# Kernel optimization log

Hardware: AMD Instinct MI355X
Metric: run time of the kernel (lower is better)

Reference implementation:

```python
import jax, jax.numpy as jnp
import numpy as np

BIG = 1e9  # self-distance masking constant, as in the torch module


def setup_inputs() -> dict:
    key = jax.random.key(0)
    k1, _ = jax.random.split(key)
    coords = jax.random.normal(k1, (8, 4096, 3), dtype=jnp.float32)
    mask = jnp.ones((8, 4096), dtype=bool)
    return {"coords": coords, "mask": mask}


def reference(coords, mask):
    # coords: [B, N, 3]; mask is accepted but unused (matches the torch module)
    B, N, _ = coords.shape
    # Pairwise Euclidean distances via the |a|^2 + |b|^2 - 2ab identity
    # (avoids materializing the [B,N,N,3] diff tensor the torch code builds).
    sq = jnp.sum(coords * coords, axis=-1)                      # [B, N]
    inner = jnp.einsum('bnd,bmd->bnm', coords, coords)          # [B, N, N]
    d2 = sq[:, :, None] + sq[:, None, :] - 2.0 * inner
    dist = jnp.sqrt(jnp.maximum(d2, 0.0))                       # [B, N, N]
    dist = dist + jnp.eye(N, dtype=dist.dtype) * BIG            # mask self
    # argsort(dim=2)[:, :, :2] == indices of the two smallest distances
    _, idx = jax.lax.top_k(-dist, 2)                            # [B, N, 2]
    first_nearest_indices = idx[:, :, 0]
    second_nearest_indices = idx[:, :, 1]
    A = jnp.take_along_axis(
        coords, jnp.broadcast_to(first_nearest_indices[:, :, None], (B, N, 3)), axis=1)
    C = jnp.take_along_axis(
        coords, jnp.broadcast_to(second_nearest_indices[:, :, None], (B, N, 3)), axis=1)
    return (A, C, first_nearest_indices, second_nearest_indices)
```

## Files before the change

kernel.cpp:

```cpp
#include <hip/hip_runtime.h>

#define BATCH 8
#define NPTS 4096
#define TOTQ (BATCH * NPTS)
#define TPB 256
#define BIGD 1e30f

__device__ __forceinline__ void top2min(float k, int m,
                                        float& b1, int& i1,
                                        float& b2, int& i2) {
    bool c1 = k < b1;
    bool c2 = k < b2;
    int ni2 = c2 ? m : i2;
    i2 = c1 ? i1 : ni2;
    i1 = c1 ? m : i1;
    b2 = fminf(fmaxf(k, b1), b2);
    b1 = fminf(k, b1);
}

template <int CHUNKSZ, int Q, bool EXC>
__device__ __forceinline__ void scan_loop(const float4* __restrict__ pts, int mbase,
                                          const int* nq,
                                          const float* xn, const float* yn, const float* zn,
                                          float* b1, int* i1, float* b2, int* i2) {
    for (int p = 0; p < CHUNKSZ; p += 8) {
        float4 c[8];
#pragma unroll
        for (int j = 0; j < 8; ++j) c[j] = pts[p + j];
#pragma unroll
        for (int j = 0; j < 8; ++j) {
            const int m = mbase + p + j;
#pragma unroll
            for (int q = 0; q < Q; ++q) {
                float k = fmaf(c[j].x, xn[q], fmaf(c[j].y, yn[q], fmaf(c[j].z, zn[q], c[j].w)));
                if (EXC) k = (m == nq[q]) ? BIGD : k;
                top2min(k, m, b1[q], i1[q], b2[q], i2[q]);
            }
        }
    }
}

template <int NCHUNKS, int Q>
__global__ __launch_bounds__(TPB) void knn_scan(const float* __restrict__ coords,
                                                float4* __restrict__ partial) {
    constexpr int CHUNKSZ = NPTS / NCHUNKS;
    __shared__ float4 pts[CHUNKSZ];
    const int tid   = (int)threadIdx.x;
    const int tile  = blockIdx.x;
    const int chunk = blockIdx.y;
    const int b     = blockIdx.z;
    const float* cb = coords + (size_t)b * NPTS * 3;
    const int mbase = chunk * CHUNKSZ;

    for (int p = tid; p < CHUNKSZ; p += TPB) {
        float x = cb[(mbase + p) * 3 + 0];
        float y = cb[(mbase + p) * 3 + 1];
        float z = cb[(mbase + p) * 3 + 2];
        pts[p] = make_float4(-2.0f * x, -2.0f * y, -2.0f * z, x * x + y * y + z * z);
    }

    const int qbase = tile * (TPB * Q);
    int nq[Q];
    float xn[Q], yn[Q], zn[Q], b1[Q], b2[Q];
    int i1[Q], i2[Q];
#pragma unroll
    for (int q = 0; q < Q; ++q) {
        int n = qbase + q * TPB + tid;
        nq[q] = n;
        xn[q] = cb[n * 3 + 0];
        yn[q] = cb[n * 3 + 1];
        zn[q] = cb[n * 3 + 2];
        b1[q] = BIGD; b2[q] = BIGD; i1[q] = 0; i2[q] = 0;
    }
    __syncthreads();

    const int qend = qbase + TPB * Q;
    const int mend = mbase + CHUNKSZ;
    if (mbase < qend && qbase < mend) {
        scan_loop<CHUNKSZ, Q, true >(pts, mbase, nq, xn, yn, zn, b1, i1, b2, i2);
    } else {
        scan_loop<CHUNKSZ, Q, false>(pts, mbase, nq, xn, yn, zn, b1, i1, b2, i2);
    }

#pragma unroll
    for (int q = 0; q < Q; ++q) {
        int n = qbase + q * TPB + tid;
        partial[(size_t)chunk * TOTQ + (size_t)b * NPTS + n] =
            make_float4(b1[q], __int_as_float(i1[q]), b2[q], __int_as_float(i2[q]));
    }
}

template <int NCHUNKS>
__global__ __launch_bounds__(TPB) void knn_merge(const float* __restrict__ coords,
                                                 const float4* __restrict__ partial,
                                                 float* __restrict__ out) {
    const int q = blockIdx.x * TPB + (int)threadIdx.x;
    const int b = q >> 12;
    float b1 = BIGD, b2 = BIGD;
    int i1 = 0, i2 = 0;
#pragma unroll
    for (int c = 0; c < NCHUNKS; ++c) {
        float4 pc = partial[(size_t)c * TOTQ + q];
        top2min(pc.x, __float_as_int(pc.y), b1, i1, b2, i2);
        top2min(pc.z, __float_as_int(pc.w), b1, i1, b2, i2);
    }
    const float* cb = coords + (size_t)b * NPTS * 3;
    float* A  = out;
    float* C  = out + (size_t)TOTQ * 3;
    float* I1 = out + (size_t)2 * TOTQ * 3;
    float* I2 = I1 + (size_t)TOTQ;

    A[(size_t)q * 3 + 0] = cb[i1 * 3 + 0];
    A[(size_t)q * 3 + 1] = cb[i1 * 3 + 1];
    A[(size_t)q * 3 + 2] = cb[i1 * 3 + 2];
    C[(size_t)q * 3 + 0] = cb[i2 * 3 + 0];
    C[(size_t)q * 3 + 1] = cb[i2 * 3 + 1];
    C[(size_t)q * 3 + 2] = cb[i2 * 3 + 2];
    I1[q] = (float)i1;
    I2[q] = (float)i2;
}

__global__ __launch_bounds__(TPB) void knn_full(const float* __restrict__ coords,
                                                float* __restrict__ out) {
    __shared__ float4 pts[NPTS];
    const int tid  = (int)threadIdx.x;
    const int tile = blockIdx.x;
    const int b    = blockIdx.y;
    const float* cb = coords + (size_t)b * NPTS * 3;

    for (int p = tid; p < NPTS; p += TPB) {
        float x = cb[p * 3 + 0];
        float y = cb[p * 3 + 1];
        float z = cb[p * 3 + 2];
        pts[p] = make_float4(-2.0f * x, -2.0f * y, -2.0f * z, x * x + y * y + z * z);
    }
    const int n = tile * TPB + tid;
    const float xn = cb[n * 3 + 0];
    const float yn = cb[n * 3 + 1];
    const float zn = cb[n * 3 + 2];
    __syncthreads();

    float b1 = BIGD, b2 = BIGD;
    int i1 = 0, i2 = 0;
    for (int p = 0; p < NPTS; p += 4) {
#pragma unroll
        for (int j = 0; j < 4; ++j) {
            float4 c = pts[p + j];
            float k = fmaf(c.x, xn, fmaf(c.y, yn, fmaf(c.z, zn, c.w)));
            k = (p + j == n) ? BIGD : k;
            top2min(k, p + j, b1, i1, b2, i2);
        }
    }

    const int q = b * NPTS + n;
    float* A  = out;
    float* C  = out + (size_t)TOTQ * 3;
    float* I1 = out + (size_t)2 * TOTQ * 3;
    float* I2 = I1 + (size_t)TOTQ;
    float4 p1 = pts[i1];
    float4 p2 = pts[i2];
    A[(size_t)q * 3 + 0] = -0.5f * p1.x;
    A[(size_t)q * 3 + 1] = -0.5f * p1.y;
    A[(size_t)q * 3 + 2] = -0.5f * p1.z;
    C[(size_t)q * 3 + 0] = -0.5f * p2.x;
    C[(size_t)q * 3 + 1] = -0.5f * p2.y;
    C[(size_t)q * 3 + 2] = -0.5f * p2.z;
    I1[q] = (float)i1;
    I2[q] = (float)i2;
}

extern "C" void kernel_launch(void* const* d_in, const int* in_sizes, int n_in,
                              void* d_out, int out_size, void* d_ws, size_t ws_size,
                              hipStream_t stream) {
    const float* coords = (const float*)d_in[0];
    float* out = (float*)d_out;
    float4* partial = (float4*)d_ws;
    const size_t chunk_bytes = (size_t)TOTQ * sizeof(float4);

    if (ws_size >= 32 * chunk_bytes) {
        hipLaunchKernelGGL((knn_scan<32, 4>), dim3(4, 32, BATCH), dim3(TPB), 0, stream,
                           coords, partial);
        hipLaunchKernelGGL((knn_merge<32>), dim3(TOTQ / TPB), dim3(TPB), 0, stream,
                           coords, partial, out);
    } else if (ws_size >= 16 * chunk_bytes) {
        hipLaunchKernelGGL((knn_scan<16, 4>), dim3(4, 16, BATCH), dim3(TPB), 0, stream,
                           coords, partial);
        hipLaunchKernelGGL((knn_merge<16>), dim3(TOTQ / TPB), dim3(TPB), 0, stream,
                           coords, partial, out);
    } else if (ws_size >= 8 * chunk_bytes) {
        hipLaunchKernelGGL((knn_scan<8, 2>), dim3(8, 8, BATCH), dim3(TPB), 0, stream,
                           coords, partial);
        hipLaunchKernelGGL((knn_merge<8>), dim3(TOTQ / TPB), dim3(TPB), 0, stream,
                           coords, partial, out);
    } else if (ws_size >= 4 * chunk_bytes) {
        hipLaunchKernelGGL((knn_scan<4, 1>), dim3(16, 4, BATCH), dim3(TPB), 0, stream,
                           coords, partial);
        hipLaunchKernelGGL((knn_merge<4>), dim3(TOTQ / TPB), dim3(TPB), 0, stream,
                           coords, partial, out);
    } else {
        hipLaunchKernelGGL(knn_full, dim3(NPTS / TPB, BATCH), dim3(TPB), 0, stream,
                           coords, out);
    }
}
```

Baseline: 107.0 us.

## Track only top-2 values in scan, rescan winning chunks to recover indices

```diff
diff --git a/kernel.cpp b/kernel.cpp
--- a/kernel.cpp
+++ b/kernel.cpp
@@ -5,6 +5,14 @@
 #define TOTQ (BATCH * NPTS)
 #define TPB 256
 #define BIGD 1e30f
+
+__device__ __forceinline__ float cand_w(float x, float y, float z) {
+    return fmaf(x, x, fmaf(y, y, z * z));
+}
+__device__ __forceinline__ float cand_key(float cx, float cy, float cz, float w,
+                                          float xn, float yn, float zn) {
+    return fmaf(cx, xn, fmaf(cy, yn, fmaf(cz, zn, w)));
+}
 
 __device__ __forceinline__ void top2min(float k, int m,
                                         float& b1, int& i1,
@@ -18,106 +26,135 @@
     b1 = fminf(k, b1);
 }
 
-template <int CHUNKSZ, int Q, bool EXC>
-__device__ __forceinline__ void scan_loop(const float4* __restrict__ pts, int mbase,
-                                          const int* nq,
-                                          const float* xn, const float* yn, const float* zn,
-                                          float* b1, int* i1, float* b2, int* i2) {
-    for (int p = 0; p < CHUNKSZ; p += 8) {
-        float4 c[8];
-#pragma unroll
-        for (int j = 0; j < 8; ++j) c[j] = pts[p + j];
-#pragma unroll
-        for (int j = 0; j < 8; ++j) {
-            const int m = mbase + p + j;
-#pragma unroll
-            for (int q = 0; q < Q; ++q) {
-                float k = fmaf(c[j].x, xn[q], fmaf(c[j].y, yn[q], fmaf(c[j].z, zn[q], c[j].w)));
-                if (EXC) k = (m == nq[q]) ? BIGD : k;
-                top2min(k, m, b1[q], i1[q], b2[q], i2[q]);
-            }
-        }
-    }
-}
-
 template <int NCHUNKS, int Q>
-__global__ __launch_bounds__(TPB) void knn_scan(const float* __restrict__ coords,
-                                                float4* __restrict__ partial) {
+__global__ __launch_bounds__(TPB, 4) void knn_scan(const float* __restrict__ coords,
+                                                   float2* __restrict__ partial) {
     constexpr int CHUNKSZ = NPTS / NCHUNKS;
     __shared__ float4 pts[CHUNKSZ];
     const int tid   = (int)threadIdx.x;
     const int tile  = blockIdx.x;
     const int chunk = blockIdx.y;
     const int b     = blockIdx.z;
-    const float* cb = coords + (size_t)b * NPTS * 3;
+    const float* basep = coords + (size_t)b * NPTS * 3;
     const int mbase = chunk * CHUNKSZ;
 
     for (int p = tid; p < CHUNKSZ; p += TPB) {
-        float x = cb[(mbase + p) * 3 + 0];
-        float y = cb[(mbase + p) * 3 + 1];
-        float z = cb[(mbase + p) * 3 + 2];
-        pts[p] = make_float4(-2.0f * x, -2.0f * y, -2.0f * z, x * x + y * y + z * z);
+        float x = basep[(mbase + p) * 3 + 0];
+        float y = basep[(mbase + p) * 3 + 1];
+        float z = basep[(mbase + p) * 3 + 2];
+        pts[p] = make_float4(-2.0f * x, -2.0f * y, -2.0f * z, cand_w(x, y, z));
     }
 
     const int qbase = tile * (TPB * Q);
-    int nq[Q];
     float xn[Q], yn[Q], zn[Q], b1[Q], b2[Q];
-    int i1[Q], i2[Q];
 #pragma unroll
     for (int q = 0; q < Q; ++q) {
         int n = qbase + q * TPB + tid;
-        nq[q] = n;
-        xn[q] = cb[n * 3 + 0];
-        yn[q] = cb[n * 3 + 1];
-        zn[q] = cb[n * 3 + 2];
-        b1[q] = BIGD; b2[q] = BIGD; i1[q] = 0; i2[q] = 0;
+        xn[q] = basep[n * 3 + 0];
+        yn[q] = basep[n * 3 + 1];
+        zn[q] = basep[n * 3 + 2];
+        b1[q] = BIGD; b2[q] = BIGD;
     }
     __syncthreads();
 
-    const int qend = qbase + TPB * Q;
-    const int mend = mbase + CHUNKSZ;
-    if (mbase < qend && qbase < mend) {
-        scan_loop<CHUNKSZ, Q, true >(pts, mbase, nq, xn, yn, zn, b1, i1, b2, i2);
-    } else {
-        scan_loop<CHUNKSZ, Q, false>(pts, mbase, nq, xn, yn, zn, b1, i1, b2, i2);
+    for (int p = 0; p < CHUNKSZ; p += 8) {
+        float4 c[8];
+#pragma unroll
+        for (int j = 0; j < 8; ++j) c[j] = pts[p + j];
+#pragma unroll
+        for (int j = 0; j < 8; ++j) {
+#pragma unroll
+            for (int q = 0; q < Q; ++q) {
+                float k = cand_key(c[j].x, c[j].y, c[j].z, c[j].w, xn[q], yn[q], zn[q]);
+                b2[q] = fminf(fmaxf(k, b1[q]), b2[q]);
+                b1[q] = fminf(k, b1[q]);
+            }
+        }
     }
 
 #pragma unroll
     for (int q = 0; q < Q; ++q) {
         int n = qbase + q * TPB + tid;
-        partial[(size_t)chunk * TOTQ + (size_t)b * NPTS + n] =
-            make_float4(b1[q], __int_as_float(i1[q]), b2[q], __int_as_float(i2[q]));
+        partial[(size_t)chunk * TOTQ + (size_t)b * NPTS + n] = make_float2(b1[q], b2[q]);
+    }
+}
+
+template <int CHUNKSZ>
+__device__ __forceinline__ void rescan_chunk(const float* __restrict__ basep, int c, int n,
+                                             float xn, float yn, float zn,
+                                             float& r1, int& j1, float& r2, int& j2) {
+    r1 = BIGD; r2 = BIGD; j1 = 0; j2 = 0;
+    const int m0 = c * CHUNKSZ;
+    for (int m = m0; m < m0 + CHUNKSZ; ++m) {
+        float x = basep[m * 3 + 0];
+        float y = basep[m * 3 + 1];
+        float z = basep[m * 3 + 2];
+        float w = cand_w(x, y, z);
+        float k = cand_key(-2.0f * x, -2.0f * y, -2.0f * z, w, xn, yn, zn);
+        k = (m == n) ? BIGD : k;
+        top2min(k, m, r1, j1, r2, j2);
     }
 }
 
 template <int NCHUNKS>
 __global__ __launch_bounds__(TPB) void knn_merge(const float* __restrict__ coords,
-                                                 const float4* __restrict__ partial,
+                                                 const float2* __restrict__ partial,
                                                  float* __restrict__ out) {
+    constexpr int CHUNKSZ = NPTS / NCHUNKS;
     const int q = blockIdx.x * TPB + (int)threadIdx.x;
     const int b = q >> 12;
-    float b1 = BIGD, b2 = BIGD;
-    int i1 = 0, i2 = 0;
-#pragma unroll
+    const int n = q & (NPTS - 1);
+    const float* basep = coords + (size_t)b * NPTS * 3;
+    const int c_self = n / CHUNKSZ;
+
+    const float xn = basep[n * 3 + 0];
+    const float yn = basep[n * 3 + 1];
+    const float zn = basep[n * 3 + 2];
+
+    float v1 = BIGD, v2 = BIGD;
+    int ca = (c_self == 0) ? 1 : 0, cbk = ca;
     for (int c = 0; c < NCHUNKS; ++c) {
-        float4 pc = partial[(size_t)c * TOTQ + q];
-        top2min(pc.x, __float_as_int(pc.y), b1, i1, b2, i2);
-        top2min(pc.z, __float_as_int(pc.w), b1, i1, b2, i2);
-    }
-    const float* cb = coords + (size_t)b * NPTS * 3;
+        if (c == c_self) continue;
+        float2 v = partial[(size_t)c * TOTQ + q];
+        top2min(v.x, c, v1, ca, v2, cbk);
+        top2min(v.y, c, v1, ca, v2, cbk);
+    }
+
+    int lo3 = min(min(c_self, ca), cbk);
+    int hi3 = max(max(c_self, ca), cbk);
+    int md3 = c_self + ca + cbk - lo3 - hi3;
+
+    float f1 = BIGD, f2 = BIGD;
+    int g1 = 0, g2 = 0;
+    float r1, r2; int j1, j2;
+
+    rescan_chunk<CHUNKSZ>(basep, lo3, n, xn, yn, zn, r1, j1, r2, j2);
+    top2min(r1, j1, f1, g1, f2, g2);
+    top2min(r2, j2, f1, g1, f2, g2);
+    if (md3 > lo3) {
+        rescan_chunk<CHUNKSZ>(basep, md3, n, xn, yn, zn, r1, j1, r2, j2);
+        top2min(r1, j1, f1, g1, f2, g2);
+        top2min(r2, j2, f1, g1, f2, g2);
+    }
+    if (hi3 > md3) {
+        rescan_chunk<CHUNKSZ>(basep, hi3, n, xn, yn, zn, r1, j1, r2, j2);
+        top2min(r1, j1, f1, g1, f2, g2);
+        top2min(r2, j2, f1, g1, f2, g2);
+    }
+
     float* A  = out;
     float* C  = out + (size_t)TOTQ * 3;
     float* I1 = out + (size_t)2 * TOTQ * 3;
     float* I2 = I1 + (size_t)TOTQ;
 
-    A[(size_t)q * 3 + 0] = cb[i1 * 3 + 0];
-    A[(size_t)q * 3 + 1] = cb[i1 * 3 + 1];
-    A[(size_t)q * 3 + 2] = cb[i1 * 3 + 2];
-    C[(size_t)q * 3 + 0] = cb[i2 * 3 + 0];
-    C[(size_t)q * 3 + 1] = cb[i2 * 3 + 1];
-    C[(size_t)q * 3 + 2] = cb[i2 * 3 + 2];
-    I1[q] = (float)i1;
-    I2[q] = (float)i2;
+    A[(size_t)q * 3 + 0] = basep[g1 * 3 + 0];
+    A[(size_t)q * 3 + 1] = basep[g1 * 3 + 1];
+    A[(size_t)q * 3 + 2] = basep[g1 * 3 + 2];
+    C[(size_t)q * 3 + 0] = basep[g2 * 3 + 0];
+    C[(size_t)q * 3 + 1] = basep[g2 * 3 + 1];
+    C[(size_t)q * 3 + 2] = basep[g2 * 3 + 2];
+    I1[q] = (float)g1;
+    I2[q] = (float)g2;
 }
 
 __global__ __launch_bounds__(TPB) void knn_full(const float* __restrict__ coords,
@@ -126,18 +163,18 @@
     const int tid  = (int)threadIdx.x;
     const int tile = blockIdx.x;
     const int b    = blockIdx.y;
-    const float* cb = coords + (size_t)b * NPTS * 3;
+    const float* basep = coords + (size_t)b * NPTS * 3;
 
     for (int p = tid; p < NPTS; p += TPB) {
-        float x = cb[p * 3 + 0];
-        float y = cb[p * 3 + 1];
-        float z = cb[p * 3 + 2];
-        pts[p] = make_float4(-2.0f * x, -2.0f * y, -2.0f * z, x * x + y * y + z * z);
+        float x = basep[p * 3 + 0];
+        float y = basep[p * 3 + 1];
+        float z = basep[p * 3 + 2];
+        pts[p] = make_float4(-2.0f * x, -2.0f * y, -2.0f * z, cand_w(x, y, z));
     }
     const int n = tile * TPB + tid;
-    const float xn = cb[n * 3 + 0];
-    const float yn = cb[n * 3 + 1];
-    const float zn = cb[n * 3 + 2];
+    const float xn = basep[n * 3 + 0];
+    const float yn = basep[n * 3 + 1];
+    const float zn = basep[n * 3 + 2];
     __syncthreads();
 
     float b1 = BIGD, b2 = BIGD;
@@ -146,7 +183,7 @@
 #pragma unroll
         for (int j = 0; j < 4; ++j) {
             float4 c = pts[p + j];
-            float k = fmaf(c.x, xn, fmaf(c.y, yn, fmaf(c.z, zn, c.w)));
+            float k = cand_key(c.x, c.y, c.z, c.w, xn, yn, zn);
             k = (p + j == n) ? BIGD : k;
             top2min(k, p + j, b1, i1, b2, i2);
         }
@@ -174,11 +211,16 @@
                               hipStream_t stream) {
     const float* coords = (const float*)d_in[0];
     float* out = (float*)d_out;
-    float4* partial = (float4*)d_ws;
-    const size_t chunk_bytes = (size_t)TOTQ * sizeof(float4);
-
-    if (ws_size >= 32 * chunk_bytes) {
-        hipLaunchKernelGGL((knn_scan<32, 4>), dim3(4, 32, BATCH), dim3(TPB), 0, stream,
+    float2* partial = (float2*)d_ws;
+    const size_t chunk_bytes = (size_t)TOTQ * sizeof(float2);
+
+    if (ws_size >= 64 * chunk_bytes) {
+        hipLaunchKernelGGL((knn_scan<64, 8>), dim3(2, 64, BATCH), dim3(TPB), 0, stream,
+                           coords, partial);
+        hipLaunchKernelGGL((knn_merge<64>), dim3(TOTQ / TPB), dim3(TPB), 0, stream,
+                           coords, partial, out);
+    } else if (ws_size >= 32 * chunk_bytes) {
+        hipLaunchKernelGGL((knn_scan<32, 8>), dim3(2, 32, BATCH), dim3(TPB), 0, stream,
                            coords, partial);
         hipLaunchKernelGGL((knn_merge<32>), dim3(TOTQ / TPB), dim3(TPB), 0, stream,
                            coords, partial, out);
@@ -187,16 +229,6 @@
                            coords, partial);
         hipLaunchKernelGGL((knn_merge<16>), dim3(TOTQ / TPB), dim3(TPB), 0, stream,
                            coords, partial, out);
-    } else if (ws_size >= 8 * chunk_bytes) {
-        hipLaunchKernelGGL((knn_scan<8, 2>), dim3(8, 8, BATCH), dim3(TPB), 0, stream,
-                           coords, partial);
-        hipLaunchKernelGGL((knn_merge<8>), dim3(TOTQ / TPB), dim3(TPB), 0, stream,
-                           coords, partial, out);
-    } else if (ws_size >= 4 * chunk_bytes) {
-        hipLaunchKernelGGL((knn_scan<4, 1>), dim3(16, 4, BATCH), dim3(TPB), 0, stream,
-                           coords, partial);
-        hipLaunchKernelGGL((knn_merge<4>), dim3(TOTQ / TPB), dim3(TPB), 0, stream,
-                           coords, partial, out);
     } else {
         hipLaunchKernelGGL(knn_full, dim3(NPTS / TPB, BATCH), dim3(TPB), 0, stream,
                            coords, out);
```

Measured after the change: 117.1 us. 1.09x slower.
